# Kernel tuning notes

Hardware: AMD Instinct MI355X
Metric: run time of the kernel (lower is better)

## Reference

```python
import math
import jax, jax.numpy as jnp
from jax import lax
import numpy as np

C, H, W, N, K = 256, 64, 64, 16, 7

def setup_inputs() -> dict:
    key = jax.random.key(0)
    k0, k1, k2, k3, k4 = jax.random.split(key, 5)
    x = jax.random.normal(k0, (N, C, H, W), dtype=jnp.float32)
    p_2_w = 0.02 * jax.random.normal(k1, (1, C, H, 1), dtype=jnp.float32)
    # nn.Conv2d(c, c, (1,5), groups=1, bias=False) -> weight [c, c, 1, 5]
    fan_in = C * 1 * 5
    bound = 1.0 / math.sqrt(fan_in)
    p_3_w = jax.random.uniform(k2, (C, C, 1, 5), dtype=jnp.float32, minval=-bound, maxval=bound)
    p_4_w = 0.02 * jax.random.normal(k3, (1, C, K, 1, 1), dtype=jnp.float32)
    p_6_w = jax.random.uniform(k4, (K, 1), dtype=jnp.float32, minval=-7.0, maxval=7.0)
    return {"x": x, "p_2_w": p_2_w, "p_3_w": p_3_w, "p_4_w": p_4_w, "p_6_w": p_6_w}

def reference(x, p_2_w, p_3_w, p_4_w, p_6_w):
    n, c, h, w = x.shape
    k = p_4_w.shape[2]  # 7 taps
    pad = (k - 1) // 2
    # F.unfold with kernel (1,7), pad (0,3): stack 7 width-shifted copies -> [n,c,7,h,w]
    xp = jnp.pad(x, ((0, 0), (0, 0), (0, 0), (pad, pad)))
    t_1 = jnp.stack([xp[..., i:i + w] for i in range(k)], axis=2)
    # per-(channel,row) scaling then dense 1x5 conv
    t_2 = p_2_w * x
    t_3 = lax.conv_general_dilated(
        t_2, p_3_w, window_strides=(1, 1), padding=[(0, 0), (2, 2)],
        dimension_numbers=("NCHW", "OIHW", "NCHW"))
    # weighted tap-sum: (p_4_w * t_1) contracted over taps with p_6_w[:,0]
    t_4 = p_4_w * t_1
    t_6 = jnp.einsum("nckhw,kf->ncfhw", t_4, p_6_w)[:, :, 0]  # [n,c,h,w]
    t_5 = jax.nn.relu(x)
    s = h * w
    # channel-attention matrix [n,c,c]
    t_7 = jnp.einsum("ncs,nds->ncd", t_3.reshape(n, c, s), t_6.reshape(n, c, s))
    t_7 = t_7 * (1.0 / math.sqrt(s))
    # bmm(t_5^T, t_7) -> [n,s,d]; permuting to [n,d,h,w] == einsum 'ncs,ncd->nds'
    out = jnp.einsum("ncs,ncd->nds", t_5.reshape(n, c, s), t_7)
    out = out * (1.0 / math.sqrt(c))
    return out.reshape(n, c, h, w)
```

## Files before the change

kernel.cpp:

```cpp
#include <hip/hip_runtime.h>
#include <hip/hip_bf16.h>

typedef __attribute__((ext_vector_type(8))) short bf16x8;
typedef __attribute__((ext_vector_type(4))) float f32x4;

#define NB 16
#define CD 256
#define HD 64
#define WD 64
#define WP 68
#define SD 4096
#define KU 1280

__device__ __forceinline__ void gload16(const void* g, void* lds) {
  __builtin_amdgcn_global_load_lds(
      (const __attribute__((address_space(1))) unsigned int*)g,
      (__attribute__((address_space(3))) unsigned int*)lds, 16, 0, 0);
}

__global__ __launch_bounds__(256) void prep_w3(const float* __restrict__ p3,
                                               __hip_bfloat16* __restrict__ A) {
  int id = blockIdx.x * 256 + threadIdx.x;
  if (id >= CD * KU) return;
  int o = id / KU;
  int r = id - o * KU;
  int j = r >> 8;
  int c = r & 255;
  A[id] = __float2bfloat16(p3[(o * CD + c) * 5 + j]);
}

__global__ __launch_bounds__(256) void prep_x(const float* __restrict__ x,
                                              const float* __restrict__ p2,
                                              const float* __restrict__ p4,
                                              const float* __restrict__ p6,
                                              __hip_bfloat16* __restrict__ t2p,
                                              __hip_bfloat16* __restrict__ t5T,
                                              __hip_bfloat16* __restrict__ t6) {
  int h = blockIdx.x;
  int c0 = blockIdx.y * 64;
  int n = blockIdx.z;
  __shared__ float xl[64][67];
  __shared__ float p2l[64];
  __shared__ float wtl[64][8];
  int t = threadIdx.x;

  if (t < 64) p2l[t] = p2[(c0 + t) * HD + h];
  for (int idx = t; idx < 448; idx += 256) {
    int c = idx / 7, k = idx - c * 7;
    wtl[c][k] = p4[(c0 + c) * 7 + k] * p6[k];
  }

  {
    int cq = t >> 4;
    int w4 = (t & 15) * 4;
#pragma unroll
    for (int cc = 0; cc < 4; ++cc) {
      int cl = cc * 16 + cq;
      const float4 xv = *reinterpret_cast<const float4*>(
          &x[(((size_t)n * CD + c0 + cl) * HD + h) * WD + w4]);
      xl[cl][w4 + 0] = xv.x;
      xl[cl][w4 + 1] = xv.y;
      xl[cl][w4 + 2] = xv.z;
      xl[cl][w4 + 3] = xv.w;
    }
  }
  __syncthreads();

  __hip_bfloat16* t2pn = t2p + (size_t)n * HD * WP * CD;
#pragma unroll
  for (int ii = 0; ii < 2; ++ii) {
    int w = (t >> 3) + ii * 32;
    int cb = (t & 7) * 8;
    __hip_bfloat16 o2[8], o5[8];
#pragma unroll
    for (int j = 0; j < 8; ++j) {
      float xv = xl[cb + j][w];
      o5[j] = __float2bfloat16(fmaxf(xv, 0.f));
      o2[j] = __float2bfloat16(p2l[cb + j] * xv);
    }
    size_t s = (size_t)h * 64 + w;
    *reinterpret_cast<bf16x8*>(&t5T[((size_t)n * SD + s) * CD + c0 + cb]) =
        *reinterpret_cast<const bf16x8*>(o5);
    *reinterpret_cast<bf16x8*>(&t2pn[((size_t)h * WP + w + 2) * CD + c0 + cb]) =
        *reinterpret_cast<const bf16x8*>(o2);
  }
  if (t < 32) {
    int pi = t >> 3;
    int wp = (pi < 2) ? pi : pi + 64;
    int cb = (t & 7) * 8;
    bf16x8 z = (bf16x8){0, 0, 0, 0, 0, 0, 0, 0};
    *reinterpret_cast<bf16x8*>(&t2pn[((size_t)h * WP + wp) * CD + c0 + cb]) = z;
  }

#pragma unroll
  for (int ii = 0; ii < 2; ++ii) {
    int cl = (t >> 3) + ii * 32;
    int w8 = (t & 7) * 8;
    float hx[14];
#pragma unroll
    for (int m = 0; m < 14; ++m) {
      int wi = w8 - 3 + m;
      hx[m] = (wi >= 0 && wi < 64) ? xl[cl][wi] : 0.f;
    }
    float wt[7];
#pragma unroll
    for (int k = 0; k < 7; ++k) wt[k] = wtl[cl][k];
    __hip_bfloat16 o6[8];
#pragma unroll
    for (int u = 0; u < 8; ++u) {
      float acc = 0.f;
#pragma unroll
      for (int k = 0; k < 7; ++k) acc += wt[k] * hx[u + k];
      o6[u] = __float2bfloat16(acc);
    }
    *reinterpret_cast<bf16x8*>(&t6[((size_t)n * CD + c0 + cl) * SD + h * 64 + w8]) =
        *reinterpret_cast<const bf16x8*>(o6);
  }
}

#define STAGE_A(c, kt, d)                                                              \
  gload16(Ab + (size_t)((c) * 64 + wv * 8 + (lane >> 3)) * 2560 + (kt) * 128 + cbsrc,  \
          (char*)lds + (d) * 65536 + (c) * 8192 + wv * 1024)
#define STAGE_B(j, kt, d)                                                              \
  gload16(t2pb + (size_t)(s0 + (j) * 64 + wv * 8 + (lane >> 3) + 4 * (sb * 4 + (j))) * 512 + \
                     (kt) * 128 + cbsrc,                                               \
          (char*)lds + (d) * 65536 + 32768 + (j) * 8192 + wv * 1024)

#define LOAD_AV(d, MH)                                                                 \
  do {                                                                                 \
    const __hip_bfloat16* pA =                                                         \
        lds + (d) * 32768 + (wm * 128 + (MH) * 64 + l16) * 64;                         \
    _Pragma("unroll") for (int ks = 0; ks < 2; ++ks) {                                 \
      int cb = (ks * 32 + lg * 8) ^ lxor;                                              \
      _Pragma("unroll") for (int mf = 0; mf < 4; ++mf)                                 \
          av[ks * 4 + mf] = *reinterpret_cast<const bf16x8*>(pA + mf * 1024 + cb);     \
    }                                                                                  \
  } while (0)

#define QUADR(d, MH, NH)                                                               \
  do {                                                                                 \
    const __hip_bfloat16* pB =                                                         \
        lds + (d) * 32768 + 16384 + (wn * 64 + (NH) * 32 + l16) * 64;                  \
    bf16x8 bv[4];                                                                      \
    _Pragma("unroll") for (int ks = 0; ks < 2; ++ks) {                                 \
      int cb = (ks * 32 + lg * 8) ^ lxor;                                              \
      _Pragma("unroll") for (int nf = 0; nf < 2; ++nf)                                 \
          bv[ks * 2 + nf] = *reinterpret_cast<const bf16x8*>(pB + nf * 1024 + cb);     \
    }                                                                                  \
    __builtin_amdgcn_s_setprio(1);                                                     \
    _Pragma("unroll") for (int ks = 0; ks < 2; ++ks)                                   \
        _Pragma("unroll") for (int mf = 0; mf < 4; ++mf)                               \
            _Pragma("unroll") for (int nf = 0; nf < 2; ++nf)                           \
                acc[(MH) * 4 + mf][(NH) * 2 + nf] = __builtin_amdgcn_mfma_f32_16x16x32_bf16( \
                    av[ks * 4 + mf], bv[ks * 2 + nf], acc[(MH) * 4 + mf][(NH) * 2 + nf], \
                    0, 0, 0);                                                          \
    __builtin_amdgcn_s_setprio(0);                                                     \
  } while (0)

#define VMWAIT(N) asm volatile("s_waitcnt vmcnt(" #N ")" ::: "memory")
#define BARRIER() __builtin_amdgcn_s_barrier()

__global__ __launch_bounds__(512, 2) void gemm_b8(const __hip_bfloat16* __restrict__ A,
                                                  const __hip_bfloat16* __restrict__ t2p,
                                                  __hip_bfloat16* __restrict__ t3) {
  __shared__ __align__(16) __hip_bfloat16 lds[65536];
  const int n = blockIdx.z;
  const int sb = blockIdx.x;
  const int t = threadIdx.x;
  const int wv = t >> 6, lane = t & 63;
  const int wm = wv >> 2, wn = wv & 3;
  const int l16 = lane & 15, lg = lane >> 4;
  const int s0 = sb * 256;
  const char* Ab = (const char*)A;
  const char* t2pb = (const char*)(t2p + (size_t)n * HD * WP * CD);
  const int cbsrc = ((lane & 7) ^ (lane >> 3)) * 16;
  const int lxor = (l16 & 7) * 8;

  f32x4 acc[8][4];
#pragma unroll
  for (int i = 0; i < 8; ++i)
#pragma unroll
    for (int j = 0; j < 4; ++j) acc[i][j] = (f32x4){0.f, 0.f, 0.f, 0.f};

  bf16x8 av[8];

  STAGE_B(0, 0, 0); STAGE_B(1, 0, 0); STAGE_B(2, 0, 0); STAGE_B(3, 0, 0);
  STAGE_A(0, 0, 0); STAGE_A(2, 0, 0); STAGE_A(1, 0, 0); STAGE_A(3, 0, 0);

  for (int kt = 0; kt < 19; ++kt) {
    const int cur = kt & 1, nxt = cur ^ 1, kn = kt + 1;
    STAGE_B(0, kn, nxt); STAGE_B(1, kn, nxt);
    VMWAIT(4);
    BARRIER();
    LOAD_AV(cur, 0);
    QUADR(cur, 0, 0);
    BARRIER();
    STAGE_B(2, kn, nxt); STAGE_B(3, kn, nxt);
    BARRIER();
    QUADR(cur, 0, 1);
    BARRIER();
    STAGE_A(0, kn, nxt); STAGE_A(2, kn, nxt);
    VMWAIT(6);
    BARRIER();
    LOAD_AV(cur, 1);
    QUADR(cur, 1, 0);
    BARRIER();
    STAGE_A(1, kn, nxt); STAGE_A(3, kn, nxt);
    BARRIER();
    QUADR(cur, 1, 1);
    BARRIER();
  }
  VMWAIT(2);
  BARRIER();
  LOAD_AV(1, 0);
  QUADR(1, 0, 0);
  BARRIER();
  BARRIER();
  QUADR(1, 0, 1);
  BARRIER();
  VMWAIT(0);
  BARRIER();
  LOAD_AV(1, 1);
  QUADR(1, 1, 0);
  BARRIER();
  BARRIER();
  QUADR(1, 1, 1);
  BARRIER();

  __hip_bfloat16* t3n = t3 + (size_t)n * CD * SD;
#pragma unroll
  for (int im = 0; im < 8; ++im)
#pragma unroll
    for (int in = 0; in < 4; ++in) {
      int row0 = wm * 128 + im * 16 + lg * 4;
      int col = s0 + wn * 64 + in * 16 + l16;
#pragma unroll
      for (int r = 0; r < 4; ++r)
        t3n[(size_t)(row0 + r) * SD + col] = __float2bfloat16(acc[im][in][r]);
    }
}

__global__ __launch_bounds__(256) void gemm_c_part(const __hip_bfloat16* __restrict__ t6,
                                                   const __hip_bfloat16* __restrict__ t3,
                                                   float* __restrict__ P4) {
  __shared__ __align__(16) __hip_bfloat16 lA[64 * 64];
  __shared__ __align__(16) __hip_bfloat16 lB[64 * 64];
  int bx = blockIdx.x;
  int cbk = bx & 3, kc = bx >> 2;
  int db = blockIdx.y;
  int n = blockIdx.z;
  int t = threadIdx.x;
  int wave = t >> 6, lane = t & 63;
  int wm = wave >> 1, wn = wave & 1;
  int l16 = lane & 15, lg = lane >> 4;
  int d0 = db * 64;
  int c0 = cbk * 64;
  int kbase = kc * 1024;
  const __hip_bfloat16* An = t6 + (size_t)n * CD * SD + kbase;
  const __hip_bfloat16* Bn = t3 + (size_t)n * CD * SD + kbase;

  int srow = t >> 3;
  int scol = (t & 7) * 8;
  const __hip_bfloat16* gA0 = An + (size_t)(d0 + srow) * SD + scol;
  const __hip_bfloat16* gA1 = An + (size_t)(d0 + srow + 32) * SD + scol;
  const __hip_bfloat16* gB0 = Bn + (size_t)(c0 + srow) * SD + scol;
  const __hip_bfloat16* gB1 = Bn + (size_t)(c0 + srow + 32) * SD + scol;
  __hip_bfloat16* lAd0 = &lA[t * 8];
  __hip_bfloat16* lAd1 = &lA[t * 8 + 32 * 64];
  __hip_bfloat16* lBd0 = &lB[t * 8];
  __hip_bfloat16* lBd1 = &lB[t * 8 + 32 * 64];

  f32x4 acc[2][2];
#pragma unroll
  for (int mi = 0; mi < 2; ++mi)
#pragma unroll
    for (int ni = 0; ni < 2; ++ni) acc[mi][ni] = (f32x4){0.f, 0.f, 0.f, 0.f};

  gload16(gA0, lAd0);
  gload16(gA1, lAd1);
  gload16(gB0, lBd0);
  gload16(gB1, lBd1);

  for (int k = 0; k < 16; ++k) {
    __syncthreads();
#pragma unroll
    for (int ks = 0; ks < 2; ++ks) {
      bf16x8 a[2], b[2];
#pragma unroll
      for (int mi = 0; mi < 2; ++mi)
        a[mi] = *reinterpret_cast<const bf16x8*>(&lA[(wm * 32 + mi * 16 + l16) * 64 + ks * 32 + lg * 8]);
#pragma unroll
      for (int ni = 0; ni < 2; ++ni)
        b[ni] = *reinterpret_cast<const bf16x8*>(&lB[(wn * 32 + ni * 16 + l16) * 64 + ks * 32 + lg * 8]);
#pragma unroll
      for (int mi = 0; mi < 2; ++mi)
#pragma unroll
        for (int ni = 0; ni < 2; ++ni)
          acc[mi][ni] = __builtin_amdgcn_mfma_f32_16x16x32_bf16(a[mi], b[ni], acc[mi][ni], 0, 0, 0);
    }
    __syncthreads();
    if (k < 15) {
      int kk = (k + 1) * 64;
      gload16(gA0 + kk, lAd0);
      gload16(gA1 + kk, lAd1);
      gload16(gB0 + kk, lBd0);
      gload16(gB1 + kk, lBd1);
    }
  }

  float* Pn = P4 + ((size_t)kc * NB + n) * CD * CD;
#pragma unroll
  for (int mi = 0; mi < 2; ++mi)
#pragma unroll
    for (int ni = 0; ni < 2; ++ni) {
      int col = c0 + wn * 32 + ni * 16 + l16;
      int row0 = d0 + wm * 32 + mi * 16 + lg * 4;
#pragma unroll
      for (int r = 0; r < 4; ++r)
        Pn[(size_t)(row0 + r) * CD + col] = acc[mi][ni][r];
    }
}

__global__ __launch_bounds__(256) void reduce_P(const float* __restrict__ P4,
                                                __hip_bfloat16* __restrict__ P) {
  size_t i = ((size_t)blockIdx.x * 256 + threadIdx.x) * 4;
  const size_t stride = (size_t)NB * CD * CD;
  float4 a = *reinterpret_cast<const float4*>(P4 + i);
  float4 b = *reinterpret_cast<const float4*>(P4 + stride + i);
  float4 c = *reinterpret_cast<const float4*>(P4 + 2 * stride + i);
  float4 d = *reinterpret_cast<const float4*>(P4 + 3 * stride + i);
  __hip_bfloat16 o[4];
  o[0] = __float2bfloat16((a.x + b.x + c.x + d.x) * 0.015625f);
  o[1] = __float2bfloat16((a.y + b.y + c.y + d.y) * 0.015625f);
  o[2] = __float2bfloat16((a.z + b.z + c.z + d.z) * 0.015625f);
  o[3] = __float2bfloat16((a.w + b.w + c.w + d.w) * 0.015625f);
  *reinterpret_cast<short4*>(&P[i]) = *reinterpret_cast<const short4*>(o);
}

__global__ __launch_bounds__(256) void gemm_d(const __hip_bfloat16* __restrict__ P,
                                              const __hip_bfloat16* __restrict__ t5T,
                                              float* __restrict__ out) {
  __shared__ __align__(16) __hip_bfloat16 lA[128 * 32];
  __shared__ __align__(16) __hip_bfloat16 lB[128 * 32];
  int n = blockIdx.z;
  int db = blockIdx.y;
  int sb = blockIdx.x;
  int t = threadIdx.x;
  int wave = t >> 6, lane = t & 63;
  int wm = wave >> 1, wn = wave & 1;
  int l16 = lane & 15, lg = lane >> 4;
  int d0 = db * 128;
  int s0 = sb * 128;
  const __hip_bfloat16* An = P + (size_t)n * CD * CD;
  const __hip_bfloat16* Bn = t5T + (size_t)n * SD * CD;

  int srow = t >> 2;
  int scol = (t & 3) * 8;
  const __hip_bfloat16* gA0 = An + (size_t)(d0 + srow) * CD + scol;
  const __hip_bfloat16* gA1 = An + (size_t)(d0 + srow + 64) * CD + scol;
  const __hip_bfloat16* gB0 = Bn + (size_t)(s0 + srow) * CD + scol;
  const __hip_bfloat16* gB1 = Bn + (size_t)(s0 + srow + 64) * CD + scol;
  __hip_bfloat16* lAd0 = &lA[t * 8];
  __hip_bfloat16* lAd1 = &lA[t * 8 + 64 * 32];
  __hip_bfloat16* lBd0 = &lB[t * 8];
  __hip_bfloat16* lBd1 = &lB[t * 8 + 64 * 32];

  f32x4 acc[4][4];
#pragma unroll
  for (int mi = 0; mi < 4; ++mi)
#pragma unroll
    for (int ni = 0; ni < 4; ++ni) acc[mi][ni] = (f32x4){0.f, 0.f, 0.f, 0.f};

  gload16(gA0, lAd0);
  gload16(gA1, lAd1);
  gload16(gB0, lBd0);
  gload16(gB1, lBd1);

  for (int k = 0; k < 8; ++k) {
    __syncthreads();
    bf16x8 a[4], b[4];
#pragma unroll
    for (int mi = 0; mi < 4; ++mi)
      a[mi] = *reinterpret_cast<const bf16x8*>(&lA[(wm * 64 + mi * 16 + l16) * 32 + lg * 8]);
#pragma unroll
    for (int ni = 0; ni < 4; ++ni)
      b[ni] = *reinterpret_cast<const bf16x8*>(&lB[(wn * 64 + ni * 16 + l16) * 32 + lg * 8]);
#pragma unroll
    for (int mi = 0; mi < 4; ++mi)
#pragma unroll
      for (int ni = 0; ni < 4; ++ni)
        acc[mi][ni] = __builtin_amdgcn_mfma_f32_16x16x32_bf16(a[mi], b[ni], acc[mi][ni], 0, 0, 0);
    __syncthreads();
    if (k < 7) {
      int kk = (k + 1) * 32;
      gload16(gA0 + kk, lAd0);
      gload16(gA1 + kk, lAd1);
      gload16(gB0 + kk, lBd0);
      gload16(gB1 + kk, lBd1);
    }
  }

  float* outn = out + (size_t)n * CD * SD;
#pragma unroll
  for (int mi = 0; mi < 4; ++mi)
#pragma unroll
    for (int ni = 0; ni < 4; ++ni) {
      int col = s0 + wn * 64 + ni * 16 + l16;
      int row0 = d0 + wm * 64 + mi * 16 + lg * 4;
#pragma unroll
      for (int r = 0; r < 4; ++r)
        outn[(size_t)(row0 + r) * SD + col] = acc[mi][ni][r] * 0.0625f;
    }
}

extern "C" void kernel_launch(void* const* d_in, const int* in_sizes, int n_in,
                              void* d_out, int out_size, void* d_ws, size_t ws_size,
                              hipStream_t stream) {
  const float* x = (const float*)d_in[0];
  const float* p2 = (const float*)d_in[1];
  const float* p3 = (const float*)d_in[2];
  const float* p4 = (const float*)d_in[3];
  const float* p6 = (const float*)d_in[4];

  char* ws = (char*)d_ws;
  size_t off = 0;
  __hip_bfloat16* A = (__hip_bfloat16*)(ws + off);
  off += (size_t)CD * KU * 2;
  size_t t2p_off = off;
  __hip_bfloat16* t2p = (__hip_bfloat16*)(ws + off);
  off += (size_t)NB * HD * WP * CD * 2;
  __hip_bfloat16* t5T = (__hip_bfloat16*)(ws + off);
  off += (size_t)NB * SD * CD * 2;
  __hip_bfloat16* t6 = (__hip_bfloat16*)(ws + off);
  off += (size_t)NB * CD * SD * 2;
  __hip_bfloat16* t3 = (__hip_bfloat16*)(ws + off);
  off += (size_t)NB * CD * SD * 2;
  float* P4 = (float*)(ws + t2p_off);
  __hip_bfloat16* P = (__hip_bfloat16*)(ws + t2p_off + (size_t)4 * NB * CD * CD * 4);

  float* out = (float*)d_out;

  prep_w3<<<dim3((CD * KU + 255) / 256), 256, 0, stream>>>(p3, A);
  prep_x<<<dim3(HD, 4, NB), 256, 0, stream>>>(x, p2, p4, p6, t2p, t5T, t6);
  gemm_b8<<<dim3(16, 1, NB), 512, 0, stream>>>(A, t2p, t3);
  gemm_c_part<<<dim3(16, 4, NB), 256, 0, stream>>>(t6, t3, P4);
  reduce_P<<<dim3((NB * CD * CD / 4) / 256), 256, 0, stream>>>(P4, P);
  gemm_d<<<dim3(32, 2, NB), 256, 0, stream>>>(P, t5T, out);
}
```

Before: 137.4 us.

## Enlarge gemm_d tile to full 256 rows with 64-wide K and swizzled LDS

The final GEMM now computes all 256 d-rows per block (8x4 MFMA fragments per wave) instead of splitting d across two blocks, so each t5T tile is loaded once. The K step grows from 32 to 64, halving the barrier/load iterations, and LDS rows use an XOR swizzle to avoid bank conflicts on fragment reads. Launch bounds request 2 blocks per CU. In exchange the grid halves to 512 blocks and register pressure roughly doubles with 32 accumulators per lane.

```diff
diff --git a/kernel.cpp b/kernel.cpp
--- a/kernel.cpp
+++ b/kernel.cpp
@@ -337,79 +337,79 @@
   *reinterpret_cast<short4*>(&P[i]) = *reinterpret_cast<const short4*>(o);
 }
 
-__global__ __launch_bounds__(256) void gemm_d(const __hip_bfloat16* __restrict__ P,
-                                              const __hip_bfloat16* __restrict__ t5T,
-                                              float* __restrict__ out) {
-  __shared__ __align__(16) __hip_bfloat16 lA[128 * 32];
-  __shared__ __align__(16) __hip_bfloat16 lB[128 * 32];
-  int n = blockIdx.z;
-  int db = blockIdx.y;
-  int sb = blockIdx.x;
-  int t = threadIdx.x;
-  int wave = t >> 6, lane = t & 63;
-  int wm = wave >> 1, wn = wave & 1;
-  int l16 = lane & 15, lg = lane >> 4;
-  int d0 = db * 128;
-  int s0 = sb * 128;
-  const __hip_bfloat16* An = P + (size_t)n * CD * CD;
-  const __hip_bfloat16* Bn = t5T + (size_t)n * SD * CD;
-
-  int srow = t >> 2;
-  int scol = (t & 3) * 8;
-  const __hip_bfloat16* gA0 = An + (size_t)(d0 + srow) * CD + scol;
-  const __hip_bfloat16* gA1 = An + (size_t)(d0 + srow + 64) * CD + scol;
-  const __hip_bfloat16* gB0 = Bn + (size_t)(s0 + srow) * CD + scol;
-  const __hip_bfloat16* gB1 = Bn + (size_t)(s0 + srow + 64) * CD + scol;
-  __hip_bfloat16* lAd0 = &lA[t * 8];
-  __hip_bfloat16* lAd1 = &lA[t * 8 + 64 * 32];
-  __hip_bfloat16* lBd0 = &lB[t * 8];
-  __hip_bfloat16* lBd1 = &lB[t * 8 + 64 * 32];
-
-  f32x4 acc[4][4];
-#pragma unroll
-  for (int mi = 0; mi < 4; ++mi)
-#pragma unroll
-    for (int ni = 0; ni < 4; ++ni) acc[mi][ni] = (f32x4){0.f, 0.f, 0.f, 0.f};
-
-  gload16(gA0, lAd0);
-  gload16(gA1, lAd1);
-  gload16(gB0, lBd0);
-  gload16(gB1, lBd1);
-
-  for (int k = 0; k < 8; ++k) {
+#define DSTAGE_A(i, kk)                                                                \
+  gload16(Pb + (size_t)((i) * 32 + wv4 * 8 + (lane >> 3)) * 512 + (kk) * 128 + cbsrc,  \
+          (char*)lA + (i) * 4096 + wv4 * 1024)
+#define DSTAGE_B(i, kk)                                                                \
+  gload16(Tb + (size_t)(s0 + (i) * 32 + wv4 * 8 + (lane >> 3)) * 512 + (kk) * 128 + cbsrc, \
+          (char*)lB + (i) * 4096 + wv4 * 1024)
+
+__global__ __launch_bounds__(256, 2) void gemm_d(const __hip_bfloat16* __restrict__ P,
+                                                 const __hip_bfloat16* __restrict__ t5T,
+                                                 float* __restrict__ out) {
+  __shared__ __align__(16) __hip_bfloat16 lA[256 * 64];
+  __shared__ __align__(16) __hip_bfloat16 lB[128 * 64];
+  const int n = blockIdx.z;
+  const int sb = blockIdx.x;
+  const int t = threadIdx.x;
+  const int wv4 = t >> 6, lane = t & 63;
+  const int wm = wv4 >> 1, wn = wv4 & 1;
+  const int l16 = lane & 15, lg = lane >> 4;
+  const int s0 = sb * 128;
+  const char* Pb = (const char*)(P + (size_t)n * CD * CD);
+  const char* Tb = (const char*)(t5T + (size_t)n * SD * CD);
+  const int cbsrc = ((lane & 7) ^ (lane >> 3)) * 16;
+  const int lxor = (l16 & 7) * 8;
+
+  f32x4 acc[8][4];
+#pragma unroll
+  for (int i = 0; i < 8; ++i)
+#pragma unroll
+    for (int j = 0; j < 4; ++j) acc[i][j] = (f32x4){0.f, 0.f, 0.f, 0.f};
+
+#pragma unroll
+  for (int i = 0; i < 8; ++i) DSTAGE_A(i, 0);
+#pragma unroll
+  for (int i = 0; i < 4; ++i) DSTAGE_B(i, 0);
+
+  for (int k = 0; k < 4; ++k) {
     __syncthreads();
-    bf16x8 a[4], b[4];
-#pragma unroll
-    for (int mi = 0; mi < 4; ++mi)
-      a[mi] = *reinterpret_cast<const bf16x8*>(&lA[(wm * 64 + mi * 16 + l16) * 32 + lg * 8]);
-#pragma unroll
-    for (int ni = 0; ni < 4; ++ni)
-      b[ni] = *reinterpret_cast<const bf16x8*>(&lB[(wn * 64 + ni * 16 + l16) * 32 + lg * 8]);
-#pragma unroll
-    for (int mi = 0; mi < 4; ++mi)
-#pragma unroll
-      for (int ni = 0; ni < 4; ++ni)
-        acc[mi][ni] = __builtin_amdgcn_mfma_f32_16x16x32_bf16(a[mi], b[ni], acc[mi][ni], 0, 0, 0);
+#pragma unroll
+    for (int ks = 0; ks < 2; ++ks) {
+      int cb = (ks * 32 + lg * 8) ^ lxor;
+      bf16x8 a[8], b[4];
+#pragma unroll
+      for (int mf = 0; mf < 8; ++mf)
+        a[mf] = *reinterpret_cast<const bf16x8*>(&lA[(wm * 128 + mf * 16 + l16) * 64 + cb]);
+#pragma unroll
+      for (int nf = 0; nf < 4; ++nf)
+        b[nf] = *reinterpret_cast<const bf16x8*>(&lB[(wn * 64 + nf * 16 + l16) * 64 + cb]);
+#pragma unroll
+      for (int mf = 0; mf < 8; ++mf)
+#pragma unroll
+        for (int nf = 0; nf < 4; ++nf)
+          acc[mf][nf] = __builtin_amdgcn_mfma_f32_16x16x32_bf16(a[mf], b[nf], acc[mf][nf], 0, 0, 0);
+    }
     __syncthreads();
-    if (k < 7) {
-      int kk = (k + 1) * 32;
-      gload16(gA0 + kk, lAd0);
-      gload16(gA1 + kk, lAd1);
-      gload16(gB0 + kk, lBd0);
-      gload16(gB1 + kk, lBd1);
+    if (k < 3) {
+      int kk = k + 1;
+#pragma unroll
+      for (int i = 0; i < 8; ++i) DSTAGE_A(i, kk);
+#pragma unroll
+      for (int i = 0; i < 4; ++i) DSTAGE_B(i, kk);
     }
   }
 
   float* outn = out + (size_t)n * CD * SD;
 #pragma unroll
-  for (int mi = 0; mi < 4; ++mi)
-#pragma unroll
-    for (int ni = 0; ni < 4; ++ni) {
-      int col = s0 + wn * 64 + ni * 16 + l16;
-      int row0 = d0 + wm * 64 + mi * 16 + lg * 4;
+  for (int mf = 0; mf < 8; ++mf)
+#pragma unroll
+    for (int nf = 0; nf < 4; ++nf) {
+      int col = s0 + wn * 64 + nf * 16 + l16;
+      int row0 = wm * 128 + mf * 16 + lg * 4;
 #pragma unroll
       for (int r = 0; r < 4; ++r)
-        outn[(size_t)(row0 + r) * SD + col] = acc[mi][ni][r] * 0.0625f;
+        outn[(size_t)(row0 + r) * SD + col] = acc[mf][nf][r] * 0.0625f;
     }
 }
 
@@ -445,5 +445,5 @@
   gemm_b8<<<dim3(16, 1, NB), 512, 0, stream>>>(A, t2p, t3);
   gemm_c_part<<<dim3(16, 4, NB), 256, 0, stream>>>(t6, t3, P4);
   reduce_P<<<dim3((NB * CD * CD / 4) / 256), 256, 0, stream>>>(P4, P);
-  gemm_d<<<dim3(32, 2, NB), 256, 0, stream>>>(P, t5T, out);
-}
+  gemm_d<<<dim3(32, 1, NB), 256, 0, stream>>>(P, t5T, out);
+}
```

Measured after the change: 133.3 us. 1.03x faster.
